# Kernel tuning notes

Hardware: AMD Instinct MI355X
Metric: run time of the kernel (lower is better)

The kernel has to match this reference:

```python
import jax, jax.numpy as jnp
import numpy as np


def setup_inputs() -> dict:
    key = jax.random.key(0)
    ks = jax.random.split(key, 5)
    B, DEC, ENC, H = 4, 256, 1024, 256
    s = 1.0 / np.sqrt(H)
    return {
        "x_decoder": jax.random.normal(ks[0], (B, DEC, H), dtype=jnp.float32),
        "x_encoder": jax.random.normal(ks[1], (B, ENC, H), dtype=jnp.float32),
        "w1": jax.random.normal(ks[2], (H, H), dtype=jnp.float32) * s,
        "w2": jax.random.normal(ks[3], (H, H), dtype=jnp.float32) * s,
        "v": jax.random.normal(ks[4], (H,), dtype=jnp.float32) * s,
    }


def reference(x_decoder, x_encoder, w1, w2, v):
    # nn.Linear applies x @ W^T; weights here stored as (out, in) = (H, H)
    enc_t = jnp.einsum('beh,oh->beo', x_encoder, w1)   # (B, ENC, H)
    dec_t = jnp.einsum('bdh,oh->bdo', x_decoder, w2)   # (B, DEC, H)
    # Broadcast-add -> tanh -> dot with v: scores (B, DEC, ENC)
    scores = jnp.einsum('bdeh,h->bde',
                        jnp.tanh(dec_t[:, :, None, :] + enc_t[:, None, :, :]), v)
    return jax.nn.log_softmax(scores, axis=-1)
```

## Files before the change

### kernel.cpp

```cpp
#include <hip/hip_runtime.h>
#include <hip/hip_bf16.h>


#define B_ 4
#define DEC_ 256
#define ENC_ 1024
#define H_ 256

using bf16x8 = __attribute__((ext_vector_type(8))) short;
using f32x4 = __attribute__((ext_vector_type(4))) float;

__device__ inline short f2bf(float f) {
  union { float f; unsigned u; } x; x.f = f;
  return (short)((x.u + 0x8000u) >> 16);
}


#define LDK 72

__global__ __launch_bounds__(256) void gemm_mfma(
    const float* __restrict__ w1, const float* __restrict__ xe,
    const float* __restrict__ xd, const float* __restrict__ w2,
    float* __restrict__ encE, float* __restrict__ decE) {
  const int blk = blockIdx.x;
  const float* A;
  const float* Bsrc;
  float* C;
  int ldc, m0, n0;
  if (blk < 256) {
    const int b = blk >> 6;
    const int t = blk & 63;
    m0 = (t >> 4) << 6; n0 = (t & 15) << 6;
    A = w1;
    Bsrc = xe + (size_t)b * ENC_ * H_;
    C = encE + (size_t)b * H_ * ENC_;
    ldc = ENC_;
  } else {
    const int blk2 = blk - 256;
    const int b = blk2 >> 4;
    const int t = blk2 & 15;
    m0 = (t >> 2) << 6; n0 = (t & 3) << 6;
    A = xd + (size_t)b * DEC_ * H_;
    Bsrc = w2;
    C = decE + (size_t)b * DEC_ * H_;
    ldc = H_;
  }
  const int K = H_;
  const int tid = threadIdx.x;
  const int wave = tid >> 6, lane = tid & 63;
  const int wm = (wave >> 1) << 5, wn = (wave & 1) << 5;
  const int fr = lane & 15;
  const int fk = (lane >> 4) << 3;

  __shared__ short As[2][64][LDK];
  __shared__ short Bs[2][64][LDK];

  const int srow = tid >> 2;
  const int skq = (tid & 3) << 4;
  const float* ag = A + (size_t)(m0 + srow) * K + skq;
  const float* bg = Bsrc + (size_t)(n0 + srow) * K + skq;

  float4 ra[4], rb[4];
#define LDCHUNK(K0)                                                    \
  {                                                                    \
    _Pragma("unroll")                                                  \
    for (int i = 0; i < 4; ++i) {                                      \
      ra[i] = *(const float4*)(ag + (K0) + 4 * i);                     \
      rb[i] = *(const float4*)(bg + (K0) + 4 * i);                     \
    }                                                                  \
  }
#define STCHUNK(BUF)                                                   \
  {                                                                    \
    _Pragma("unroll")                                                  \
    for (int j = 0; j < 2; ++j) {                                      \
      bf16x8 pa, pb;                                                   \
      pa[0] = f2bf(ra[2 * j].x);     pa[1] = f2bf(ra[2 * j].y);        \
      pa[2] = f2bf(ra[2 * j].z);     pa[3] = f2bf(ra[2 * j].w);        \
      pa[4] = f2bf(ra[2 * j + 1].x); pa[5] = f2bf(ra[2 * j + 1].y);    \
      pa[6] = f2bf(ra[2 * j + 1].z); pa[7] = f2bf(ra[2 * j + 1].w);    \
      pb[0] = f2bf(rb[2 * j].x);     pb[1] = f2bf(rb[2 * j].y);        \
      pb[2] = f2bf(rb[2 * j].z);     pb[3] = f2bf(rb[2 * j].w);        \
      pb[4] = f2bf(rb[2 * j + 1].x); pb[5] = f2bf(rb[2 * j + 1].y);    \
      pb[6] = f2bf(rb[2 * j + 1].z); pb[7] = f2bf(rb[2 * j + 1].w);    \
      *(bf16x8*)&As[BUF][srow][skq + 8 * j] = pa;                      \
      *(bf16x8*)&Bs[BUF][srow][skq + 8 * j] = pb;                      \
    }                                                                  \
  }

  f32x4 acc[2][2] = {};

#define COMPUTE(BUF)                                                   \
  {                                                                    \
    _Pragma("unroll")                                                  \
    for (int kk = 0; kk < 2; ++kk) {                                   \
      bf16x8 af[2], bff[2];                                            \
      _Pragma("unroll")                                                \
      for (int mi = 0; mi < 2; ++mi)                                   \
        af[mi] = *(const bf16x8*)&As[BUF][wm + (mi << 4) + fr][(kk << 5) + fk]; \
      _Pragma("unroll")                                                \
      for (int ni = 0; ni < 2; ++ni)                                   \
        bff[ni] = *(const bf16x8*)&Bs[BUF][wn + (ni << 4) + fr][(kk << 5) + fk]; \
      _Pragma("unroll")                                                \
      for (int mi = 0; mi < 2; ++mi)                                   \
        _Pragma("unroll")                                              \
        for (int ni = 0; ni < 2; ++ni)                                 \
          acc[mi][ni] = __builtin_amdgcn_mfma_f32_16x16x32_bf16(       \
              af[mi], bff[ni], acc[mi][ni], 0, 0, 0);                  \
    }                                                                  \
  }

  LDCHUNK(0)
  STCHUNK(0)
  __syncthreads();
  LDCHUNK(64) COMPUTE(0) STCHUNK(1) __syncthreads();
  LDCHUNK(128) COMPUTE(1) STCHUNK(0) __syncthreads();
  LDCHUNK(192) COMPUTE(0) STCHUNK(1) __syncthreads();
  COMPUTE(1)

  const float SC = 2.8853900817779268f;
#pragma unroll
  for (int mi = 0; mi < 2; ++mi) {
#pragma unroll
    for (int ni = 0; ni < 2; ++ni) {
      const int row = m0 + wm + (mi << 4) + ((lane >> 4) << 2);
      const int col = n0 + wn + (ni << 4) + (lane & 15);
#pragma unroll
      for (int r = 0; r < 4; ++r)
        C[(size_t)(row + r) * ldc + col] =
            __builtin_amdgcn_exp2f(acc[mi][ni][r] * SC);
    }
  }
}


#define DT 4

#define PROC1(D4, ACC)                                                 \
  {                                                                    \
    const float m0 = fmaf(E0, (D4).x, 1.0f);                           \
    const float m1 = fmaf(E1, (D4).y, 1.0f);                           \
    const float m2 = fmaf(E2, (D4).z, 1.0f);                           \
    const float m3 = fmaf(E3, (D4).w, 1.0f);                           \
    const float pa = m0 * m1, pb = m2 * m3;                            \
    const float n01 = fmaf(wC.x, m1, wC.y * m0);                       \
    const float n23 = fmaf(wC.z, m3, wC.w * m2);                       \
    const float num = fmaf(n01, pb, n23 * pa);                         \
    ACC = fmaf(num, __builtin_amdgcn_rcpf(pa * pb), ACC);              \
  }

__global__ __launch_bounds__(1024) void scores_lsm(
    const float* __restrict__ encE, const float* __restrict__ decE,
    const float* __restrict__ v, float* __restrict__ out) {
  const int bid = blockIdx.x;
  const int xcd = bid & 7;
  const int b = xcd >> 1;
  const int d0 = ((((bid >> 3) << 1) | (xcd & 1))) * DT;
  const int tid = threadIdx.x;

  __shared__ float redv[16];
  __shared__ float redm[DT][16];
  __shared__ float reds[DT][16];

  const int lane = tid & 63;
  const int wid = tid >> 6;

  float pv = (tid < H_) ? v[tid] : 0.0f;
#pragma unroll
  for (int o = 32; o >= 1; o >>= 1) pv += __shfl_xor(pv, o, 64);
  if (lane == 0) redv[wid] = pv;
  __syncthreads();
  float vsum = 0.0f;
#pragma unroll
  for (int w = 0; w < 4; ++w) vsum += redv[w];

  const float* ep = encE + (size_t)b * H_ * ENC_ + tid;
  const float* dp = decE + (size_t)(b * DEC_ + d0) * H_;
  float acc0 = 0.0f, acc1 = 0.0f, acc2 = 0.0f, acc3 = 0.0f;

  float Ec[4], En[4];
#pragma unroll
  for (int i = 0; i < 4; ++i) Ec[i] = ep[(size_t)i * ENC_];
#pragma unroll
  for (int i = 0; i < 4; ++i) En[i] = ep[(size_t)(4 + i) * ENC_];

  float4 wC = *(const float4*)(v);
  float4 dC0 = *(const float4*)(dp);
  float4 dC1 = *(const float4*)(dp + H_);
  float4 dC2 = *(const float4*)(dp + 2 * H_);
  float4 dC3 = *(const float4*)(dp + 3 * H_);

  for (int g = 0; g < 64; ++g) {
    float Et[4] = {0.f, 0.f, 0.f, 0.f};
    if (g + 2 < 64) {
      const float* p = ep + (size_t)(4 * g + 8) * ENC_;
#pragma unroll
      for (int i = 0; i < 4; ++i) Et[i] = p[(size_t)i * ENC_];
    }
    float4 wN = wC, dN0 = dC0, dN1 = dC1, dN2 = dC2, dN3 = dC3;
    if (g < 63) {
      const int h4 = 4 * (g + 1);
      wN = *(const float4*)(v + h4);
      dN0 = *(const float4*)(dp + h4);
      dN1 = *(const float4*)(dp + H_ + h4);
      dN2 = *(const float4*)(dp + 2 * H_ + h4);
      dN3 = *(const float4*)(dp + 3 * H_ + h4);
    }
    const float E0 = Ec[0], E1 = Ec[1], E2 = Ec[2], E3 = Ec[3];
    PROC1(dC0, acc0)
    PROC1(dC1, acc1)
    PROC1(dC2, acc2)
    PROC1(dC3, acc3)
#pragma unroll
    for (int i = 0; i < 4; ++i) { Ec[i] = En[i]; En[i] = Et[i]; }
    wC = wN; dC0 = dN0; dC1 = dN1; dC2 = dN2; dC3 = dN3;
  }

  float s[DT];
  s[0] = fmaf(-2.0f, acc0, vsum);
  s[1] = fmaf(-2.0f, acc1, vsum);
  s[2] = fmaf(-2.0f, acc2, vsum);
  s[3] = fmaf(-2.0f, acc3, vsum);

  const float L2E = 1.4426950408889634f;
  const float LN2 = 0.6931471805599453f;

#pragma unroll
  for (int d = 0; d < DT; ++d) {
    float m = s[d];
#pragma unroll
    for (int o = 32; o >= 1; o >>= 1) m = fmaxf(m, __shfl_xor(m, o, 64));
    if (lane == 0) redm[d][wid] = m;
  }
  __syncthreads();

  float M[DT];
#pragma unroll
  for (int d = 0; d < DT; ++d) {
    float m = redm[d][0];
#pragma unroll
    for (int w = 1; w < 16; ++w) m = fmaxf(m, redm[d][w]);
    M[d] = m;
    float z = __builtin_amdgcn_exp2f((s[d] - m) * L2E);
#pragma unroll
    for (int o = 32; o >= 1; o >>= 1) z += __shfl_xor(z, o, 64);
    if (lane == 0) reds[d][wid] = z;
  }
  __syncthreads();

#pragma unroll
  for (int d = 0; d < DT; ++d) {
    float S = 0.0f;
#pragma unroll
    for (int w = 0; w < 16; ++w) S += reds[d][w];
    const float lse = M[d] + LN2 * __builtin_amdgcn_logf(S);
    out[(size_t)(b * DEC_ + d0 + d) * ENC_ + tid] = s[d] - lse;
  }
}

extern "C" void kernel_launch(void* const* d_in, const int* in_sizes, int n_in,
                              void* d_out, int out_size, void* d_ws, size_t ws_size,
                              hipStream_t stream) {
  const float* xd = (const float*)d_in[0];
  const float* xe = (const float*)d_in[1];
  const float* w1 = (const float*)d_in[2];
  const float* w2 = (const float*)d_in[3];
  const float* v  = (const float*)d_in[4];
  float* out = (float*)d_out;

  float* encE = (float*)d_ws;
  float* decE = encE + (size_t)B_ * H_ * ENC_;

  gemm_mfma<<<320, 256, 0, stream>>>(w1, xe, xd, w2, encE, decE);
  scores_lsm<<<B_ * (DEC_ / DT), 1024, 0, stream>>>(encE, decE, v, out);
}
```

Measured before the change: 48.11 us.

## Split fused score+log-softmax into finer-grained score kernel and separate LSE pass

Replaces the single 1024-thread score+log_softmax kernel (4 decoder rows per block, full ENC width) with a 256-thread score kernel in which each block handles 2 decoder rows over a quarter of the encoder dimension, writing raw scores. A new row-wise kernel then does log_softmax in place. The vsum constant term is dropped because it cancels in log_softmax, and the manual software prefetch is replaced by a plain unrolled loop. This gives more, smaller blocks for load balance, but adds an extra kernel launch and a full write-then-read round trip of the 4 MB output.

```diff
diff --git a/kernel.cpp b/kernel.cpp
--- a/kernel.cpp
+++ b/kernel.cpp
@@ -14,7 +14,6 @@
   union { float f; unsigned u; } x; x.f = f;
   return (short)((x.u + 0x8000u) >> 16);
 }
-
 
 #define LDK 72
 
@@ -133,8 +132,6 @@
 }
 
 
-#define DT 4
-
 #define PROC1(D4, ACC)                                                 \
   {                                                                    \
     const float m0 = fmaf(E0, (D4).x, 1.0f);                           \
@@ -148,113 +145,73 @@
     ACC = fmaf(num, __builtin_amdgcn_rcpf(pa * pb), ACC);              \
   }
 
-__global__ __launch_bounds__(1024) void scores_lsm(
+__global__ __launch_bounds__(256) void scores_k(
     const float* __restrict__ encE, const float* __restrict__ decE,
     const float* __restrict__ v, float* __restrict__ out) {
   const int bid = blockIdx.x;
   const int xcd = bid & 7;
   const int b = xcd >> 1;
-  const int d0 = ((((bid >> 3) << 1) | (xcd & 1))) * DT;
+  const int sub = ((bid >> 3) << 1) | (xcd & 1);
+  const int es = sub & 3;
+  const int d0 = (sub >> 2) << 1;
+  const int e = (es << 8) + threadIdx.x;
+
+  const float* ep = encE + (size_t)b * H_ * ENC_ + e;
+  const float* dp = decE + (size_t)(b * DEC_ + d0) * H_;
+  float acc0 = 0.0f, acc1 = 0.0f;
+
+#pragma unroll 4
+  for (int g = 0; g < 64; ++g) {
+    const int h = g << 2;
+    const float E0 = ep[(size_t)h * ENC_];
+    const float E1 = ep[(size_t)(h + 1) * ENC_];
+    const float E2 = ep[(size_t)(h + 2) * ENC_];
+    const float E3 = ep[(size_t)(h + 3) * ENC_];
+    const float4 wC = *(const float4*)(v + h);
+    const float4 dA = *(const float4*)(dp + h);
+    const float4 dB = *(const float4*)(dp + H_ + h);
+    PROC1(dA, acc0)
+    PROC1(dB, acc1)
+  }
+
+  float* orow = out + (size_t)(b * DEC_ + d0) * ENC_ + e;
+  orow[0] = -2.0f * acc0;
+  orow[ENC_] = -2.0f * acc1;
+}
+
+
+__global__ __launch_bounds__(256) void lsm_k(float* __restrict__ out) {
+  const int row = blockIdx.x;
+  float* p = out + (size_t)row * ENC_;
   const int tid = threadIdx.x;
-
-  __shared__ float redv[16];
-  __shared__ float redm[DT][16];
-  __shared__ float reds[DT][16];
-
-  const int lane = tid & 63;
-  const int wid = tid >> 6;
-
-  float pv = (tid < H_) ? v[tid] : 0.0f;
-#pragma unroll
-  for (int o = 32; o >= 1; o >>= 1) pv += __shfl_xor(pv, o, 64);
-  if (lane == 0) redv[wid] = pv;
+  const int lane = tid & 63, wid = tid >> 6;
+
+  __shared__ float rm[4], rs[4];
+
+  float4 x = *(const float4*)(p + 4 * tid);
+
+  float m = fmaxf(fmaxf(x.x, x.y), fmaxf(x.z, x.w));
+#pragma unroll
+  for (int o = 32; o >= 1; o >>= 1) m = fmaxf(m, __shfl_xor(m, o, 64));
+  if (lane == 0) rm[wid] = m;
   __syncthreads();
-  float vsum = 0.0f;
-#pragma unroll
-  for (int w = 0; w < 4; ++w) vsum += redv[w];
-
-  const float* ep = encE + (size_t)b * H_ * ENC_ + tid;
-  const float* dp = decE + (size_t)(b * DEC_ + d0) * H_;
-  float acc0 = 0.0f, acc1 = 0.0f, acc2 = 0.0f, acc3 = 0.0f;
-
-  float Ec[4], En[4];
-#pragma unroll
-  for (int i = 0; i < 4; ++i) Ec[i] = ep[(size_t)i * ENC_];
-#pragma unroll
-  for (int i = 0; i < 4; ++i) En[i] = ep[(size_t)(4 + i) * ENC_];
-
-  float4 wC = *(const float4*)(v);
-  float4 dC0 = *(const float4*)(dp);
-  float4 dC1 = *(const float4*)(dp + H_);
-  float4 dC2 = *(const float4*)(dp + 2 * H_);
-  float4 dC3 = *(const float4*)(dp + 3 * H_);
-
-  for (int g = 0; g < 64; ++g) {
-    float Et[4] = {0.f, 0.f, 0.f, 0.f};
-    if (g + 2 < 64) {
-      const float* p = ep + (size_t)(4 * g + 8) * ENC_;
-#pragma unroll
-      for (int i = 0; i < 4; ++i) Et[i] = p[(size_t)i * ENC_];
-    }
-    float4 wN = wC, dN0 = dC0, dN1 = dC1, dN2 = dC2, dN3 = dC3;
-    if (g < 63) {
-      const int h4 = 4 * (g + 1);
-      wN = *(const float4*)(v + h4);
-      dN0 = *(const float4*)(dp + h4);
-      dN1 = *(const float4*)(dp + H_ + h4);
-      dN2 = *(const float4*)(dp + 2 * H_ + h4);
-      dN3 = *(const float4*)(dp + 3 * H_ + h4);
-    }
-    const float E0 = Ec[0], E1 = Ec[1], E2 = Ec[2], E3 = Ec[3];
-    PROC1(dC0, acc0)
-    PROC1(dC1, acc1)
-    PROC1(dC2, acc2)
-    PROC1(dC3, acc3)
-#pragma unroll
-    for (int i = 0; i < 4; ++i) { Ec[i] = En[i]; En[i] = Et[i]; }
-    wC = wN; dC0 = dN0; dC1 = dN1; dC2 = dN2; dC3 = dN3;
-  }
-
-  float s[DT];
-  s[0] = fmaf(-2.0f, acc0, vsum);
-  s[1] = fmaf(-2.0f, acc1, vsum);
-  s[2] = fmaf(-2.0f, acc2, vsum);
-  s[3] = fmaf(-2.0f, acc3, vsum);
+  const float M = fmaxf(fmaxf(rm[0], rm[1]), fmaxf(rm[2], rm[3]));
 
   const float L2E = 1.4426950408889634f;
   const float LN2 = 0.6931471805599453f;
-
-#pragma unroll
-  for (int d = 0; d < DT; ++d) {
-    float m = s[d];
-#pragma unroll
-    for (int o = 32; o >= 1; o >>= 1) m = fmaxf(m, __shfl_xor(m, o, 64));
-    if (lane == 0) redm[d][wid] = m;
-  }
+  float z = __builtin_amdgcn_exp2f((x.x - M) * L2E) +
+            __builtin_amdgcn_exp2f((x.y - M) * L2E) +
+            __builtin_amdgcn_exp2f((x.z - M) * L2E) +
+            __builtin_amdgcn_exp2f((x.w - M) * L2E);
+#pragma unroll
+  for (int o = 32; o >= 1; o >>= 1) z += __shfl_xor(z, o, 64);
+  if (lane == 0) rs[wid] = z;
   __syncthreads();
-
-  float M[DT];
-#pragma unroll
-  for (int d = 0; d < DT; ++d) {
-    float m = redm[d][0];
-#pragma unroll
-    for (int w = 1; w < 16; ++w) m = fmaxf(m, redm[d][w]);
-    M[d] = m;
-    float z = __builtin_amdgcn_exp2f((s[d] - m) * L2E);
-#pragma unroll
-    for (int o = 32; o >= 1; o >>= 1) z += __shfl_xor(z, o, 64);
-    if (lane == 0) reds[d][wid] = z;
-  }
-  __syncthreads();
-
-#pragma unroll
-  for (int d = 0; d < DT; ++d) {
-    float S = 0.0f;
-#pragma unroll
-    for (int w = 0; w < 16; ++w) S += reds[d][w];
-    const float lse = M[d] + LN2 * __builtin_amdgcn_logf(S);
-    out[(size_t)(b * DEC_ + d0 + d) * ENC_ + tid] = s[d] - lse;
-  }
+  const float S = (rs[0] + rs[1]) + (rs[2] + rs[3]);
+
+  const float lse = M + LN2 * __builtin_amdgcn_logf(S);
+  x.x -= lse; x.y -= lse; x.z -= lse; x.w -= lse;
+  *(float4*)(p + 4 * tid) = x;
 }
 
 extern "C" void kernel_launch(void* const* d_in, const int* in_sizes, int n_in,
@@ -271,5 +228,6 @@
   float* decE = encE + (size_t)B_ * H_ * ENC_;
 
   gemm_mfma<<<320, 256, 0, stream>>>(w1, xe, xd, w2, encE, decE);
-  scores_lsm<<<B_ * (DEC_ / DT), 1024, 0, stream>>>(encE, decE, v, out);
-}
+  scores_k<<<2048, 256, 0, stream>>>(encE, decE, v, out);
+  lsm_k<<<B_ * DEC_, 256, 0, stream>>>(out);
+}
```

Result: faster. 45.99 us (-4.4%).
